# Optimization experiments

Hardware: AMD Instinct MI355X
Metric: run time of the kernel (lower is better)

The kernel has to match this reference:

```python
import jax, jax.numpy as jnp
import numpy as np

N = 20000      # nodes
E = 320000     # edges (before self-loops)
F_IN = 512     # input feature size
HID = 128      # encoder hidden
OUT = 128      # encoder output / GAT in_channels
H = 4          # gat heads
C = 64         # gat out_channels per head


def setup_inputs() -> dict:
    key = jax.random.key(0)
    ks = jax.random.split(key, 10)
    s = 0.05
    return {
        "x": jax.random.normal(ks[0], (N, F_IN), jnp.float32),
        "edge_index": jax.random.randint(ks[1], (2, E), 0, N, dtype=jnp.int64),
        "W1": jax.random.normal(ks[2], (F_IN, HID), jnp.float32) * s,
        "b1": jax.random.normal(ks[3], (HID,), jnp.float32) * s,
        "W2": jax.random.normal(ks[4], (HID, OUT), jnp.float32) * s,
        "b2": jax.random.normal(ks[5], (OUT,), jnp.float32) * s,
        "Wg": jax.random.normal(ks[6], (OUT, H * C), jnp.float32) * s,
        "att_src": jax.random.normal(ks[7], (H, C), jnp.float32) * s,
        "att_dst": jax.random.normal(ks[8], (H, C), jnp.float32) * s,
        "bias_g": jax.random.normal(ks[9], (H * C,), jnp.float32) * s,
    }


def reference(x, edge_index, W1, b1, W2, b2, Wg, att_src, att_dst, bias_g):
    # MLP encoder: Linear -> ReLU -> Linear
    h = jnp.maximum(x @ W1 + b1, 0.0) @ W2 + b2            # [N, OUT]

    # GATConv (concat=True, eval mode -> no dropout)
    xg = (h @ Wg).reshape(N, H, C)                          # per-head projections

    # add self-loops (PyG GATConv default)
    loops = jnp.arange(N, dtype=edge_index.dtype)
    src = jnp.concatenate([edge_index[0], loops])           # [E+N] source j
    dst = jnp.concatenate([edge_index[1], loops])           # [E+N] dest   i

    a_src = jnp.einsum('nhc,hc->nh', xg, att_src)           # [N, H]
    a_dst = jnp.einsum('nhc,hc->nh', xg, att_dst)           # [N, H]

    e = jax.nn.leaky_relu(a_src[src] + a_dst[dst], 0.2)     # [E+N, H]

    # segment softmax over incoming edges of each destination node
    m = jax.ops.segment_max(e, dst, num_segments=N)         # [N, H]
    ex = jnp.exp(e - m[dst])
    denom = jax.ops.segment_sum(ex, dst, num_segments=N)
    alpha = ex / (denom[dst] + 1e-16)                       # [E+N, H]

    # weighted scatter-add aggregation
    out = jax.ops.segment_sum(alpha[:, :, None] * xg[src], dst, num_segments=N)  # [N, H, C]
    return out.reshape(N, H * C) + bias_g
```

## Files before the change

### kernel.cpp

```cpp
#include <hip/hip_runtime.h>
#include <math.h>

#define NNODES 20000
#define NEDGES 320000
#define FIN    512
#define HIDD   128
#define OUTD   128
#define NH     4
#define NC     64
#define HC     256

typedef short bf16x8 __attribute__((ext_vector_type(8)));
typedef float f32x4  __attribute__((ext_vector_type(4)));

__device__ __forceinline__ unsigned short f2bf(float f) {
    unsigned int u = __float_as_uint(f);
    unsigned int r = 0x7fffu + ((u >> 16) & 1u);
    return (unsigned short)((u + r) >> 16);
}
__device__ __forceinline__ float b2f(short t) {
    return __uint_as_float(((unsigned)(unsigned short)t) << 16);
}
__device__ __forceinline__ float4 f4max(float4 a, float4 b) {
    return make_float4(fmaxf(a.x,b.x), fmaxf(a.y,b.y), fmaxf(a.z,b.z), fmaxf(a.w,b.w));
}
__device__ __forceinline__ float4 f4add(float4 a, float4 b) {
    return make_float4(a.x+b.x, a.y+b.y, a.z+b.z, a.w+b.w);
}
__device__ __forceinline__ float4 f4sub(float4 a, float4 b) {
    return make_float4(a.x-b.x, a.y-b.y, a.z-b.z, a.w-b.w);
}
__device__ __forceinline__ float4 f4mul(float4 a, float4 b) {
    return make_float4(a.x*b.x, a.y*b.y, a.z*b.z, a.w*b.w);
}
__device__ __forceinline__ float4 f4exp(float4 a) {
    return make_float4(__expf(a.x), __expf(a.y), __expf(a.z), __expf(a.w));
}
__device__ __forceinline__ float4 shflx4(float4 v, int m) {
    return make_float4(__shfl_xor(v.x,m), __shfl_xor(v.y,m), __shfl_xor(v.z,m), __shfl_xor(v.w,m));
}

__global__ __launch_bounds__(256)
void prep_kernel(const float* __restrict__ W1, unsigned short* __restrict__ W1t,
                 const float* __restrict__ W2, const float* __restrict__ b2,
                 const float* __restrict__ Wg, unsigned short* __restrict__ W2gt,
                 float* __restrict__ b2g, int* __restrict__ deg, int n) {
    const int T1 = FIN * HIDD;
    const int T2 = HC * HIDD;
    int idx = blockIdx.x * 256 + threadIdx.x;
    if (idx < T1) {
        int nn = idx / FIN, k = idx % FIN;
        W1t[idx] = f2bf(W1[(size_t)k * HIDD + nn]);
    } else if (idx < T1 + T2) {
        int local = idx - T1;
        int nn = local >> 7;
        int k  = local & 127;
        float s = 0.f;
        #pragma unroll 8
        for (int t = 0; t < HIDD; ++t)
            s += W2[(size_t)k * OUTD + t] * Wg[(size_t)t * HC + nn];
        W2gt[(size_t)nn * HIDD + k] = f2bf(s);
        if (k == 0) {
            float t2 = 0.f;
            #pragma unroll 8
            for (int t = 0; t < OUTD; ++t) t2 += b2[t] * Wg[(size_t)t * HC + nn];
            b2g[nn] = t2;
        }
    } else if (idx < T1 + T2 + n) {
        deg[idx - T1 - T2] = 1;
    }
}

template<bool A_IS_F32, bool OUT_BF16, int BM>
__global__ __launch_bounds__(256)
void mfma_gemm_kernel(const void* __restrict__ Aptr,
                      const unsigned short* __restrict__ Bt,
                      const float* __restrict__ bias,
                      void* __restrict__ Cptr,
                      int M, int N, int K, int do_relu) {
    constexpr int MF = BM / 32;
    __shared__ unsigned short As[BM * 64];
    __shared__ unsigned short Bs[128 * 64];

    const int tid  = threadIdx.x;
    const int lane = tid & 63;
    const int w    = tid >> 6;
    const int wr   = w >> 1;
    const int wc   = w & 1;
    const int m0   = blockIdx.x * BM;
    const int n0   = blockIdx.y * 128;

    char* pA = (char*)As;
    char* pB = (char*)Bs;

    f32x4 acc[MF][4];
    #pragma unroll
    for (int m = 0; m < MF; ++m)
        #pragma unroll
        for (int n = 0; n < 4; ++n) acc[m][n] = (f32x4){0.f, 0.f, 0.f, 0.f};

    for (int k0 = 0; k0 < K; k0 += 64) {
        if (A_IS_F32) {
            if constexpr (BM == 64) {
                const int row = tid >> 2;
                const int ks  = (tid & 3) << 4;
                const bool ok = (m0 + row) < M;
                const float4* Ap = (const float4*)((const float*)Aptr +
                                   (size_t)(m0 + row) * K + k0 + ks);
                float4 f0 = make_float4(0,0,0,0), f1 = f0, f2 = f0, f3 = f0;
                if (ok) { f0 = Ap[0]; f1 = Ap[1]; f2 = Ap[2]; f3 = Ap[3]; }
                unsigned short u[16];
                u[0]=f2bf(f0.x); u[1]=f2bf(f0.y); u[2]=f2bf(f0.z); u[3]=f2bf(f0.w);
                u[4]=f2bf(f1.x); u[5]=f2bf(f1.y); u[6]=f2bf(f1.z); u[7]=f2bf(f1.w);
                u[8]=f2bf(f2.x); u[9]=f2bf(f2.y); u[10]=f2bf(f2.z); u[11]=f2bf(f2.w);
                u[12]=f2bf(f3.x); u[13]=f2bf(f3.y); u[14]=f2bf(f3.z); u[15]=f2bf(f3.w);
                const int sw = (row & 7) << 4;
                const int base = row * 128 + ks * 2;
                *(bf16x8*)(pA + ((base     ) ^ sw)) = *(bf16x8*)&u[0];
                *(bf16x8*)(pA + ((base + 16) ^ sw)) = *(bf16x8*)&u[8];
            } else {
                const int row = tid >> 3;
                const int sg  = tid & 7;
                const bool ok = (m0 + row) < M;
                const float4* Ap = (const float4*)((const float*)Aptr +
                                   (size_t)(m0 + row) * K + k0 + sg * 8);
                float4 f0 = make_float4(0,0,0,0), f1 = f0;
                if (ok) { f0 = Ap[0]; f1 = Ap[1]; }
                unsigned short u[8];
                u[0]=f2bf(f0.x); u[1]=f2bf(f0.y); u[2]=f2bf(f0.z); u[3]=f2bf(f0.w);
                u[4]=f2bf(f1.x); u[5]=f2bf(f1.y); u[6]=f2bf(f1.z); u[7]=f2bf(f1.w);
                *(bf16x8*)(pA + (((row * 128 + sg * 16)) ^ ((row & 7) << 4))) = *(bf16x8*)&u[0];
            }
        } else {
            const unsigned short* Ab = (const unsigned short*)Aptr;
            #pragma unroll
            for (int i = 0; i < BM / 32; ++i) {
                int s   = tid + i * 256;
                int row = s >> 3;
                int sg  = s & 7;
                bf16x8 v = {};
                if ((m0 + row) < M)
                    v = *(const bf16x8*)(Ab + (size_t)(m0 + row) * K + k0 + sg * 8);
                *(bf16x8*)(pA + (((row * 128 + sg * 16)) ^ ((row & 7) << 4))) = v;
            }
        }
        #pragma unroll
        for (int i = 0; i < 4; ++i) {
            int s   = tid + i * 256;
            int col = s >> 3;
            int sg  = s & 7;
            bf16x8 v = *(const bf16x8*)(Bt + (size_t)(n0 + col) * K + k0 + sg * 8);
            *(bf16x8*)(pB + (((col * 128 + sg * 16)) ^ ((col & 7) << 4))) = v;
        }
        __syncthreads();

        #pragma unroll
        for (int ks = 0; ks < 2; ++ks) {
            const int kb = ks * 64 + ((lane >> 4) << 4);
            bf16x8 a[MF], b[4];
            #pragma unroll
            for (int m = 0; m < MF; ++m) {
                int row = wr * (16 * MF) + m * 16 + (lane & 15);
                a[m] = *(const bf16x8*)(pA + ((row * 128 + kb) ^ ((row & 7) << 4)));
            }
            #pragma unroll
            for (int n = 0; n < 4; ++n) {
                int col = wc * 64 + n * 16 + (lane & 15);
                b[n] = *(const bf16x8*)(pB + ((col * 128 + kb) ^ ((col & 7) << 4)));
            }
            #pragma unroll
            for (int m = 0; m < MF; ++m)
                #pragma unroll
                for (int n = 0; n < 4; ++n)
                    acc[m][n] = __builtin_amdgcn_mfma_f32_16x16x32_bf16(
                        a[m], b[n], acc[m][n], 0, 0, 0);
        }
        __syncthreads();
    }

    #pragma unroll
    for (int n = 0; n < 4; ++n) {
        const int col = n0 + wc * 64 + n * 16 + (lane & 15);
        const float bv = bias ? bias[col] : 0.f;
        #pragma unroll
        for (int m = 0; m < MF; ++m) {
            #pragma unroll
            for (int r = 0; r < 4; ++r) {
                const int row = m0 + wr * (16 * MF) + m * 16 + ((lane >> 4) << 2) + r;
                if (row >= M) continue;
                float v = acc[m][n][r] + bv;
                if (do_relu) v = fmaxf(v, 0.f);
                if (OUT_BF16)
                    ((unsigned short*)Cptr)[(size_t)row * N + col] = f2bf(v);
                else
                    ((float*)Cptr)[(size_t)row * N + col] = v;
            }
        }
    }
}

__global__ __launch_bounds__(256)
void dots_count_kernel(const unsigned short* __restrict__ xgb,
                       const float* __restrict__ att_src, const float* __restrict__ att_dst,
                       float* __restrict__ a_src, float* __restrict__ a_dst,
                       const int* __restrict__ dst, int* __restrict__ deg,
                       int n, int e, int nb_dots) {
    if ((int)blockIdx.x < nb_dots) {
        int idx = blockIdx.x * 256 + threadIdx.x;
        if (idx >= n * NH) return;
        int node = idx >> 2;
        int h = idx & 3;
        const bf16x8* xr = (const bf16x8*)(xgb + (size_t)node * HC + h * NC);
        const float* sa = att_src + h * NC;
        const float* da = att_dst + h * NC;
        float ss = 0.f, dd = 0.f;
        #pragma unroll
        for (int j = 0; j < 8; ++j) {
            bf16x8 v = xr[j];
            #pragma unroll
            for (int t = 0; t < 8; ++t) {
                float f = b2f(v[t]);
                ss += f * sa[j * 8 + t];
                dd += f * da[j * 8 + t];
            }
        }
        a_src[idx] = ss;
        a_dst[idx] = dd;
    } else {
        int i = (blockIdx.x - nb_dots) * 256 + threadIdx.x;
        if (i < e) atomicAdd(&deg[dst[i]], 1);
    }
}

__global__ __launch_bounds__(1024)
void scan_offsets_kernel(const int* __restrict__ deg, int* __restrict__ offs,
                         int* __restrict__ cursor, int n) {
    __shared__ int wsum[16], wbase[16];
    const int tid = threadIdx.x, lane = tid & 63, w = tid >> 6;
    const int i0 = tid * 20;
    int loc[20];
    int s = 0;
    #pragma unroll
    for (int k = 0; k < 20; ++k) {
        int i = i0 + k;
        int v = (i < n) ? deg[i] : 0;
        loc[k] = s;
        s += v;
    }
    int incl = s;
    #pragma unroll
    for (int d = 1; d < 64; d <<= 1) {
        int t = __shfl_up(incl, d);
        if (lane >= d) incl += t;
    }
    if (lane == 63) wsum[w] = incl;
    __syncthreads();
    if (w == 0) {
        int v = (lane < 16) ? wsum[lane] : 0;
        int sc = v;
        #pragma unroll
        for (int d = 1; d < 16; d <<= 1) {
            int t = __shfl_up(sc, d);
            if (lane >= d) sc += t;
        }
        if (lane < 16) wbase[lane] = sc - v;
    }
    __syncthreads();
    const int excl = wbase[w] + incl - s;
    #pragma unroll
    for (int k = 0; k < 20; ++k) {
        int i = i0 + k;
        if (i < n) { int o = excl + loc[k]; offs[i] = o; cursor[i] = o; }
    }
    if (tid == 1023) offs[n] = excl + s;
}

__global__ void scatter_kernel(const int* __restrict__ src, const int* __restrict__ dst,
                               int* __restrict__ cursor, int* __restrict__ csr_src,
                               int e, int n) {
    int i = blockIdx.x * 256 + threadIdx.x;
    if (i < e) {
        int s = src[i], d = dst[i];
        csr_src[atomicAdd(&cursor[d], 1)] = s;
    } else if (i < e + n) {
        int node = i - e;
        csr_src[atomicAdd(&cursor[node], 1)] = node;
    }
}

__global__ __launch_bounds__(256)
void gat_aggregate3_kernel(const unsigned short* __restrict__ xgb,
                           const float4* __restrict__ asrc4,
                           const float4* __restrict__ adst4,
                           const int* __restrict__ offs, const int* __restrict__ csr_src,
                           const float* __restrict__ bias, float* __restrict__ out, int n) {
    __shared__ float4 exbuf[4][64];
    __shared__ int    sbuf[4][64];
    const int wv   = threadIdx.x >> 6;
    const int lane = threadIdx.x & 63;
    const int node = blockIdx.x * 4 + wv;
    if (node >= n) return;
    const int beg = offs[node], end = offs[node + 1];
    const int deg = end - beg;
    const float4 adstv = adst4[node];

    float4 m   = make_float4(-INFINITY, -INFINITY, -INFINITY, -INFINITY);
    float4 den = make_float4(0.f, 0.f, 0.f, 0.f);
    for (int c0 = 0; c0 < deg; c0 += 64) {
        int idx = beg + c0 + lane;
        bool ok = idx < end;
        int s = ok ? csr_src[idx] : 0;
        float4 e = make_float4(-INFINITY, -INFINITY, -INFINITY, -INFINITY);
        if (ok) {
            float4 a = asrc4[s];
            e = f4add(a, adstv);
            e.x = e.x > 0.f ? e.x : 0.2f * e.x;
            e.y = e.y > 0.f ? e.y : 0.2f * e.y;
            e.z = e.z > 0.f ? e.z : 0.2f * e.z;
            e.w = e.w > 0.f ? e.w : 0.2f * e.w;
        }
        float4 cm = e;
        #pragma unroll
        for (int dd = 32; dd >= 1; dd >>= 1) cm = f4max(cm, shflx4(cm, dd));
        float4 nm = f4max(m, cm);
        float4 ex = f4exp(f4sub(e, nm));
        exbuf[wv][lane] = ex;
        sbuf[wv][lane]  = s;
        float4 cs = ex;
        #pragma unroll
        for (int dd = 32; dd >= 1; dd >>= 1) cs = f4add(cs, shflx4(cs, dd));
        den = f4add(f4mul(den, f4exp(f4sub(m, nm))), cs);
        m = nm;
    }

    const int hi = lane >> 5;
    const int ll = lane & 31;
    const int h  = ll >> 3;
    const float denh = (h == 0) ? den.x : (h == 1) ? den.y : (h == 2) ? den.z : den.w;
    const float inv = 1.f / (denh + 1e-16f);

    float4 acc0 = make_float4(0.f, 0.f, 0.f, 0.f);
    float4 acc1 = make_float4(0.f, 0.f, 0.f, 0.f);
    const float* exf = (const float*)&exbuf[wv][0];

    auto do_edge = [&](int jj) {
        int s = sbuf[wv][jj];
        float wgt = exf[jj * 4 + h];
        bf16x8 v = *(const bf16x8*)(xgb + (size_t)s * HC + ll * 8);
        acc0.x += wgt * b2f(v[0]); acc0.y += wgt * b2f(v[1]);
        acc0.z += wgt * b2f(v[2]); acc0.w += wgt * b2f(v[3]);
        acc1.x += wgt * b2f(v[4]); acc1.y += wgt * b2f(v[5]);
        acc1.z += wgt * b2f(v[6]); acc1.w += wgt * b2f(v[7]);
    };

    auto run_chunk = [&](int cn) {
        int j = 0;
        for (; j + 8 <= cn; j += 8) {
            int j0 = j + hi, j1 = j + 2 + hi, j2 = j + 4 + hi, j3 = j + 6 + hi;
            int s0 = sbuf[wv][j0], s1 = sbuf[wv][j1], s2 = sbuf[wv][j2], s3 = sbuf[wv][j3];
            float w0 = exf[j0*4+h], w1 = exf[j1*4+h], w2 = exf[j2*4+h], w3 = exf[j3*4+h];
            bf16x8 v0 = *(const bf16x8*)(xgb + (size_t)s0 * HC + ll * 8);
            bf16x8 v1 = *(const bf16x8*)(xgb + (size_t)s1 * HC + ll * 8);
            bf16x8 v2 = *(const bf16x8*)(xgb + (size_t)s2 * HC + ll * 8);
            bf16x8 v3 = *(const bf16x8*)(xgb + (size_t)s3 * HC + ll * 8);
            acc0.x += w0*b2f(v0[0]); acc0.y += w0*b2f(v0[1]); acc0.z += w0*b2f(v0[2]); acc0.w += w0*b2f(v0[3]);
            acc1.x += w0*b2f(v0[4]); acc1.y += w0*b2f(v0[5]); acc1.z += w0*b2f(v0[6]); acc1.w += w0*b2f(v0[7]);
            acc0.x += w1*b2f(v1[0]); acc0.y += w1*b2f(v1[1]); acc0.z += w1*b2f(v1[2]); acc0.w += w1*b2f(v1[3]);
            acc1.x += w1*b2f(v1[4]); acc1.y += w1*b2f(v1[5]); acc1.z += w1*b2f(v1[6]); acc1.w += w1*b2f(v1[7]);
            acc0.x += w2*b2f(v2[0]); acc0.y += w2*b2f(v2[1]); acc0.z += w2*b2f(v2[2]); acc0.w += w2*b2f(v2[3]);
            acc1.x += w2*b2f(v2[4]); acc1.y += w2*b2f(v2[5]); acc1.z += w2*b2f(v2[6]); acc1.w += w2*b2f(v2[7]);
            acc0.x += w3*b2f(v3[0]); acc0.y += w3*b2f(v3[1]); acc0.z += w3*b2f(v3[2]); acc0.w += w3*b2f(v3[3]);
            acc1.x += w3*b2f(v3[4]); acc1.y += w3*b2f(v3[5]); acc1.z += w3*b2f(v3[6]); acc1.w += w3*b2f(v3[7]);
        }
        for (; j + 4 <= cn; j += 4) {
            do_edge(j + hi);
            do_edge(j + 2 + hi);
        }
        for (; j < cn; j += 2) {
            int jj = j + hi;
            if (jj < cn) do_edge(jj);
        }
    };

    if (deg <= 64) {
        run_chunk(deg);
    } else {
        for (int c0 = 0; c0 < deg; c0 += 64) {
            int idx = beg + c0 + lane;
            if (idx < end) {
                int s = csr_src[idx];
                float4 e = f4add(asrc4[s], adstv);
                e.x = e.x > 0.f ? e.x : 0.2f * e.x;
                e.y = e.y > 0.f ? e.y : 0.2f * e.y;
                e.z = e.z > 0.f ? e.z : 0.2f * e.z;
                e.w = e.w > 0.f ? e.w : 0.2f * e.w;
                exbuf[wv][lane] = f4exp(f4sub(e, m));
                sbuf[wv][lane]  = s;
            }
            int cn = deg - c0; if (cn > 64) cn = 64;
            run_chunk(cn);
        }
    }

    acc0.x += __shfl_xor(acc0.x, 32); acc0.y += __shfl_xor(acc0.y, 32);
    acc0.z += __shfl_xor(acc0.z, 32); acc0.w += __shfl_xor(acc0.w, 32);
    acc1.x += __shfl_xor(acc1.x, 32); acc1.y += __shfl_xor(acc1.y, 32);
    acc1.z += __shfl_xor(acc1.z, 32); acc1.w += __shfl_xor(acc1.w, 32);

    const float4* b4 = (const float4*)bias;
    float4* op = (float4*)(out + (size_t)node * HC);
    if (hi == 0) {
        float4 bv = b4[ll * 2];
        op[ll * 2] = make_float4(acc0.x * inv + bv.x, acc0.y * inv + bv.y,
                                 acc0.z * inv + bv.z, acc0.w * inv + bv.w);
    } else {
        float4 bv = b4[ll * 2 + 1];
        op[ll * 2 + 1] = make_float4(acc1.x * inv + bv.x, acc1.y * inv + bv.y,
                                     acc1.z * inv + bv.z, acc1.w * inv + bv.w);
    }
}

extern "C" void kernel_launch(void* const* d_in, const int* in_sizes, int n_in,
                              void* d_out, int out_size, void* d_ws, size_t ws_size,
                              hipStream_t stream) {
    const float* x       = (const float*)d_in[0];
    const int*   ei      = (const int*)d_in[1];
    const float* W1      = (const float*)d_in[2];
    const float* b1      = (const float*)d_in[3];
    const float* W2      = (const float*)d_in[4];
    const float* b2      = (const float*)d_in[5];
    const float* Wg      = (const float*)d_in[6];
    const float* att_src = (const float*)d_in[7];
    const float* att_dst = (const float*)d_in[8];
    const float* bias_g  = (const float*)d_in[9];

    const int Nn = in_sizes[0] / FIN;
    const int E  = in_sizes[1] / 2;
    const int* e_src = ei;
    const int* e_dst = ei + E;

    char* w = (char*)d_ws;
    auto alloc = [&](size_t bytes) { char* p = w; w += (bytes + 255) & ~(size_t)255; return p; };
    unsigned short* W1t  = (unsigned short*)alloc((size_t)OUTD * FIN * 2);
    unsigned short* W2gt = (unsigned short*)alloc((size_t)HC * HIDD * 2);
    float* b2g  = (float*)alloc(HC * 4);
    unsigned short* h1  = (unsigned short*)alloc((size_t)Nn * HIDD * 2);
    unsigned short* xgb = (unsigned short*)alloc((size_t)Nn * HC * 2);
    float* asrc = (float*)alloc((size_t)Nn * NH * 4);
    float* adst = (float*)alloc((size_t)Nn * NH * 4);
    int* deg    = (int*)alloc((size_t)Nn * 4);
    int* offs   = (int*)alloc((size_t)(Nn + 1) * 4);
    int* cursor = (int*)alloc((size_t)Nn * 4);
    int* csr    = (int*)alloc((size_t)(E + Nn) * 4);

    dim3 blk(256);

    {
        int total = FIN * HIDD + HC * HIDD + Nn;
        prep_kernel<<<dim3((total + 255) / 256), blk, 0, stream>>>(
            W1, W1t, W2, b2, Wg, W2gt, b2g, deg, Nn);
    }

    mfma_gemm_kernel<true, true, 32><<<dim3((Nn + 31) / 32, 1), blk, 0, stream>>>(
        x, W1t, b1, h1, Nn, HIDD, FIN, 1);
    mfma_gemm_kernel<false, true, 64><<<dim3((Nn + 63) / 64, 2), blk, 0, stream>>>(
        h1, W2gt, b2g, xgb, Nn, HC, HIDD, 0);

    {
        int nb_dots = (Nn * NH + 255) / 256;
        int nb_cnt  = (E + 255) / 256;
        dots_count_kernel<<<dim3(nb_dots + nb_cnt), blk, 0, stream>>>(
            xgb, att_src, att_dst, asrc, adst, e_dst, deg, Nn, E, nb_dots);
    }

    scan_offsets_kernel<<<dim3(1), dim3(1024), 0, stream>>>(deg, offs, cursor, Nn);
    scatter_kernel<<<dim3((E + Nn + 255) / 256), blk, 0, stream>>>(
        e_src, e_dst, cursor, csr, E, Nn);

    gat_aggregate3_kernel<<<dim3((Nn + 3) / 4), blk, 0, stream>>>(
        xgb, (const float4*)asrc, (const float4*)adst, offs, csr, bias_g,
        (float*)d_out, Nn);
}
```

Baseline: 130.1 us.

## Fuse attention dots into second GEMM epilogue and degree count into first GEMM

The attention-score dot products are now computed in the epilogue of the second GEMM from fp32 accumulators with a shuffle reduction, which removes a separate kernel that re-read xgb. The edge degree counting moves into the first GEMM launch as extra blocks, so one launch is saved. The aggregation loop also gains a 16-edge unrolled path that issues 8 gathers at once for more memory-level parallelism. The attention dots now use unrounded fp32 values instead of the bf16-stored ones, which slightly changes numerics, and the deeper unroll raises register pressure.

```diff
diff --git a/kernel.cpp b/kernel.cpp
--- a/kernel.cpp
+++ b/kernel.cpp
@@ -71,85 +71,55 @@
     }
 }
 
-template<bool A_IS_F32, bool OUT_BF16, int BM>
 __global__ __launch_bounds__(256)
-void mfma_gemm_kernel(const void* __restrict__ Aptr,
-                      const unsigned short* __restrict__ Bt,
-                      const float* __restrict__ bias,
-                      void* __restrict__ Cptr,
-                      int M, int N, int K, int do_relu) {
-    constexpr int MF = BM / 32;
-    __shared__ unsigned short As[BM * 64];
+void gemm1_count_kernel(const float* __restrict__ A,
+                        const unsigned short* __restrict__ Bt,
+                        const float* __restrict__ bias,
+                        unsigned short* __restrict__ C,
+                        const int* __restrict__ dst, int* __restrict__ deg,
+                        int M, int E, int gemmBlocks) {
+    __shared__ unsigned short As[32 * 64];
     __shared__ unsigned short Bs[128 * 64];
+
+    if ((int)blockIdx.x >= gemmBlocks) {
+        int i = ((int)blockIdx.x - gemmBlocks) * 256 + threadIdx.x;
+        if (i < E) atomicAdd(&deg[dst[i]], 1);
+        return;
+    }
 
     const int tid  = threadIdx.x;
     const int lane = tid & 63;
     const int w    = tid >> 6;
     const int wr   = w >> 1;
     const int wc   = w & 1;
-    const int m0   = blockIdx.x * BM;
-    const int n0   = blockIdx.y * 128;
+    const int m0   = blockIdx.x * 32;
 
     char* pA = (char*)As;
     char* pB = (char*)Bs;
 
-    f32x4 acc[MF][4];
-    #pragma unroll
-    for (int m = 0; m < MF; ++m)
-        #pragma unroll
-        for (int n = 0; n < 4; ++n) acc[m][n] = (f32x4){0.f, 0.f, 0.f, 0.f};
-
-    for (int k0 = 0; k0 < K; k0 += 64) {
-        if (A_IS_F32) {
-            if constexpr (BM == 64) {
-                const int row = tid >> 2;
-                const int ks  = (tid & 3) << 4;
-                const bool ok = (m0 + row) < M;
-                const float4* Ap = (const float4*)((const float*)Aptr +
-                                   (size_t)(m0 + row) * K + k0 + ks);
-                float4 f0 = make_float4(0,0,0,0), f1 = f0, f2 = f0, f3 = f0;
-                if (ok) { f0 = Ap[0]; f1 = Ap[1]; f2 = Ap[2]; f3 = Ap[3]; }
-                unsigned short u[16];
-                u[0]=f2bf(f0.x); u[1]=f2bf(f0.y); u[2]=f2bf(f0.z); u[3]=f2bf(f0.w);
-                u[4]=f2bf(f1.x); u[5]=f2bf(f1.y); u[6]=f2bf(f1.z); u[7]=f2bf(f1.w);
-                u[8]=f2bf(f2.x); u[9]=f2bf(f2.y); u[10]=f2bf(f2.z); u[11]=f2bf(f2.w);
-                u[12]=f2bf(f3.x); u[13]=f2bf(f3.y); u[14]=f2bf(f3.z); u[15]=f2bf(f3.w);
-                const int sw = (row & 7) << 4;
-                const int base = row * 128 + ks * 2;
-                *(bf16x8*)(pA + ((base     ) ^ sw)) = *(bf16x8*)&u[0];
-                *(bf16x8*)(pA + ((base + 16) ^ sw)) = *(bf16x8*)&u[8];
-            } else {
-                const int row = tid >> 3;
-                const int sg  = tid & 7;
-                const bool ok = (m0 + row) < M;
-                const float4* Ap = (const float4*)((const float*)Aptr +
-                                   (size_t)(m0 + row) * K + k0 + sg * 8);
-                float4 f0 = make_float4(0,0,0,0), f1 = f0;
-                if (ok) { f0 = Ap[0]; f1 = Ap[1]; }
-                unsigned short u[8];
-                u[0]=f2bf(f0.x); u[1]=f2bf(f0.y); u[2]=f2bf(f0.z); u[3]=f2bf(f0.w);
-                u[4]=f2bf(f1.x); u[5]=f2bf(f1.y); u[6]=f2bf(f1.z); u[7]=f2bf(f1.w);
-                *(bf16x8*)(pA + (((row * 128 + sg * 16)) ^ ((row & 7) << 4))) = *(bf16x8*)&u[0];
-            }
-        } else {
-            const unsigned short* Ab = (const unsigned short*)Aptr;
-            #pragma unroll
-            for (int i = 0; i < BM / 32; ++i) {
-                int s   = tid + i * 256;
-                int row = s >> 3;
-                int sg  = s & 7;
-                bf16x8 v = {};
-                if ((m0 + row) < M)
-                    v = *(const bf16x8*)(Ab + (size_t)(m0 + row) * K + k0 + sg * 8);
-                *(bf16x8*)(pA + (((row * 128 + sg * 16)) ^ ((row & 7) << 4))) = v;
-            }
+    f32x4 acc[4];
+    #pragma unroll
+    for (int n = 0; n < 4; ++n) acc[n] = (f32x4){0.f, 0.f, 0.f, 0.f};
+
+    for (int k0 = 0; k0 < FIN; k0 += 64) {
+        {
+            const int row = tid >> 3;
+            const int sg  = tid & 7;
+            const bool ok = (m0 + row) < M;
+            const float4* Ap = (const float4*)(A + (size_t)(m0 + row) * FIN + k0 + sg * 8);
+            float4 f0 = make_float4(0,0,0,0), f1 = f0;
+            if (ok) { f0 = Ap[0]; f1 = Ap[1]; }
+            unsigned short u[8];
+            u[0]=f2bf(f0.x); u[1]=f2bf(f0.y); u[2]=f2bf(f0.z); u[3]=f2bf(f0.w);
+            u[4]=f2bf(f1.x); u[5]=f2bf(f1.y); u[6]=f2bf(f1.z); u[7]=f2bf(f1.w);
+            *(bf16x8*)(pA + (((row * 128 + sg * 16)) ^ ((row & 7) << 4))) = *(bf16x8*)&u[0];
         }
         #pragma unroll
         for (int i = 0; i < 4; ++i) {
             int s   = tid + i * 256;
             int col = s >> 3;
             int sg  = s & 7;
-            bf16x8 v = *(const bf16x8*)(Bt + (size_t)(n0 + col) * K + k0 + sg * 8);
+            bf16x8 v = *(const bf16x8*)(Bt + (size_t)col * FIN + k0 + sg * 8);
             *(bf16x8*)(pB + (((col * 128 + sg * 16)) ^ ((col & 7) << 4))) = v;
         }
         __syncthreads();
@@ -157,19 +127,101 @@
         #pragma unroll
         for (int ks = 0; ks < 2; ++ks) {
             const int kb = ks * 64 + ((lane >> 4) << 4);
-            bf16x8 a[MF], b[4];
-            #pragma unroll
-            for (int m = 0; m < MF; ++m) {
-                int row = wr * (16 * MF) + m * 16 + (lane & 15);
-                a[m] = *(const bf16x8*)(pA + ((row * 128 + kb) ^ ((row & 7) << 4)));
-            }
+            int row = wr * 16 + (lane & 15);
+            bf16x8 a = *(const bf16x8*)(pA + ((row * 128 + kb) ^ ((row & 7) << 4)));
+            bf16x8 b[4];
             #pragma unroll
             for (int n = 0; n < 4; ++n) {
                 int col = wc * 64 + n * 16 + (lane & 15);
                 b[n] = *(const bf16x8*)(pB + ((col * 128 + kb) ^ ((col & 7) << 4)));
             }
             #pragma unroll
-            for (int m = 0; m < MF; ++m)
+            for (int n = 0; n < 4; ++n)
+                acc[n] = __builtin_amdgcn_mfma_f32_16x16x32_bf16(a, b[n], acc[n], 0, 0, 0);
+        }
+        __syncthreads();
+    }
+
+    #pragma unroll
+    for (int n = 0; n < 4; ++n) {
+        const int col = wc * 64 + n * 16 + (lane & 15);
+        const float bv = bias[col];
+        #pragma unroll
+        for (int r = 0; r < 4; ++r) {
+            const int row = m0 + wr * 16 + ((lane >> 4) << 2) + r;
+            if (row >= M) continue;
+            float v = fmaxf(acc[n][r] + bv, 0.f);
+            C[(size_t)row * HIDD + col] = f2bf(v);
+        }
+    }
+}
+
+__global__ __launch_bounds__(256)
+void gemm2_dots_kernel(const unsigned short* __restrict__ Ab,
+                       const unsigned short* __restrict__ Bt,
+                       const float* __restrict__ b2g,
+                       const float* __restrict__ att_src,
+                       const float* __restrict__ att_dst,
+                       unsigned short* __restrict__ xgb,
+                       float* __restrict__ a_src, float* __restrict__ a_dst,
+                       int M) {
+    __shared__ unsigned short As[64 * 64];
+    __shared__ unsigned short Bs[128 * 64];
+
+    const int tid  = threadIdx.x;
+    const int lane = tid & 63;
+    const int w    = tid >> 6;
+    const int wr   = w >> 1;
+    const int wc   = w & 1;
+    const int m0   = blockIdx.x * 64;
+    const int n0   = blockIdx.y * 128;
+
+    char* pA = (char*)As;
+    char* pB = (char*)Bs;
+
+    f32x4 acc[2][4];
+    #pragma unroll
+    for (int m = 0; m < 2; ++m)
+        #pragma unroll
+        for (int n = 0; n < 4; ++n) acc[m][n] = (f32x4){0.f, 0.f, 0.f, 0.f};
+
+    for (int k0 = 0; k0 < HIDD; k0 += 64) {
+        #pragma unroll
+        for (int i = 0; i < 2; ++i) {
+            int s   = tid + i * 256;
+            int row = s >> 3;
+            int sg  = s & 7;
+            bf16x8 v = {};
+            if ((m0 + row) < M)
+                v = *(const bf16x8*)(Ab + (size_t)(m0 + row) * HIDD + k0 + sg * 8);
+            *(bf16x8*)(pA + (((row * 128 + sg * 16)) ^ ((row & 7) << 4))) = v;
+        }
+        #pragma unroll
+        for (int i = 0; i < 4; ++i) {
+            int s   = tid + i * 256;
+            int col = s >> 3;
+            int sg  = s & 7;
+            bf16x8 v = *(const bf16x8*)(Bt + (size_t)(n0 + col) * HIDD + k0 + sg * 8);
+            *(bf16x8*)(pB + (((col * 128 + sg * 16)) ^ ((col & 7) << 4))) = v;
+        }
+        __syncthreads();
+
+        #pragma unroll
+        for (int ks = 0; ks < 2; ++ks) {
+            const int kb = ks * 64 + ((lane >> 4) << 4);
+            bf16x8 a[2], b[4];
+            #pragma unroll
+            for (int m = 0; m < 2; ++m) {
+                int row = wr * 32 + m * 16 + (lane & 15);
+                a[m] = *(const bf16x8*)(pA + ((row * 128 + kb) ^ ((row & 7) << 4)));
+            }
+            #pragma unroll
+            for (int n = 0; n < 4; ++n) {
+                int col = wc * 64 + n * 16 + (lane & 15);
+                b[n] = *(const bf16x8*)(pB + ((col * 128 + kb) ^ ((col & 7) << 4)));
+            }
+            #pragma unroll
+            for (int m = 0; m < 2; ++m)
                 #pragma unroll
                 for (int n = 0; n < 4; ++n)
                     acc[m][n] = __builtin_amdgcn_mfma_f32_16x16x32_bf16(
@@ -178,57 +230,50 @@
         __syncthreads();
     }
 
+    const int head = blockIdx.y * 2 + wc;
+    const int cIn  = lane & 15;
+    float ds_p[2][4], dd_p[2][4];
+    #pragma unroll
+    for (int m = 0; m < 2; ++m)
+        #pragma unroll
+        for (int r = 0; r < 4; ++r) { ds_p[m][r] = 0.f; dd_p[m][r] = 0.f; }
+
     #pragma unroll
     for (int n = 0; n < 4; ++n) {
-        const int col = n0 + wc * 64 + n * 16 + (lane & 15);
-        const float bv = bias ? bias[col] : 0.f;
-        #pragma unroll
-        for (int m = 0; m < MF; ++m) {
+        const int ch  = n * 16 + cIn;
+        const int col = n0 + wc * 64 + n * 16 + cIn;
+        const float bv   = b2g[col];
+        const float as_c = att_src[head * NC + ch];
+        const float ad_c = att_dst[head * NC + ch];
+        #pragma unroll
+        for (int m = 0; m < 2; ++m) {
             #pragma unroll
             for (int r = 0; r < 4; ++r) {
-                const int row = m0 + wr * (16 * MF) + m * 16 + ((lane >> 4) << 2) + r;
-                if (row >= M) continue;
+                const int row = m0 + wr * 32 + m * 16 + ((lane >> 4) << 2) + r;
                 float v = acc[m][n][r] + bv;
-                if (do_relu) v = fmaxf(v, 0.f);
-                if (OUT_BF16)
-                    ((unsigned short*)Cptr)[(size_t)row * N + col] = f2bf(v);
-                else
-                    ((float*)Cptr)[(size_t)row * N + col] = v;
-            }
-        }
-    }
-}
-
-__global__ __launch_bounds__(256)
-void dots_count_kernel(const unsigned short* __restrict__ xgb,
-                       const float* __restrict__ att_src, const float* __restrict__ att_dst,
-                       float* __restrict__ a_src, float* __restrict__ a_dst,
-                       const int* __restrict__ dst, int* __restrict__ deg,
-                       int n, int e, int nb_dots) {
-    if ((int)blockIdx.x < nb_dots) {
-        int idx = blockIdx.x * 256 + threadIdx.x;
-        if (idx >= n * NH) return;
-        int node = idx >> 2;
-        int h = idx & 3;
-        const bf16x8* xr = (const bf16x8*)(xgb + (size_t)node * HC + h * NC);
-        const float* sa = att_src + h * NC;
-        const float* da = att_dst + h * NC;
-        float ss = 0.f, dd = 0.f;
-        #pragma unroll
-        for (int j = 0; j < 8; ++j) {
-            bf16x8 v = xr[j];
-            #pragma unroll
-            for (int t = 0; t < 8; ++t) {
-                float f = b2f(v[t]);
-                ss += f * sa[j * 8 + t];
-                dd += f * da[j * 8 + t];
-            }
-        }
-        a_src[idx] = ss;
-        a_dst[idx] = dd;
-    } else {
-        int i = (blockIdx.x - nb_dots) * 256 + threadIdx.x;
-        if (i < e) atomicAdd(&deg[dst[i]], 1);
+                if (row < M) xgb[(size_t)row * HC + col] = f2bf(v);
+                ds_p[m][r] += v * as_c;
+                dd_p[m][r] += v * ad_c;
+            }
+        }
+    }
+    #pragma unroll
+    for (int m = 0; m < 2; ++m) {
+        #pragma unroll
+        for (int r = 0; r < 4; ++r) {
+            float s = ds_p[m][r], d = dd_p[m][r];
+            s += __shfl_xor(s, 1); s += __shfl_xor(s, 2);
+            s += __shfl_xor(s, 4); s += __shfl_xor(s, 8);
+            d += __shfl_xor(d, 1); d += __shfl_xor(d, 2);
+            d += __shfl_xor(d, 4); d += __shfl_xor(d, 8);
+            if (cIn == 0) {
+                const int row = m0 + wr * 32 + m * 16 + ((lane >> 4) << 2) + r;
+                if (row < M) {
+                    a_src[row * NH + head] = s;
+                    a_dst[row * NH + head] = d;
+                }
+            }
+        }
     }
 }
 
@@ -289,7 +334,7 @@
 }
 
 __global__ __launch_bounds__(256)
-void gat_aggregate3_kernel(const unsigned short* __restrict__ xgb,
+void gat_aggregate4_kernel(const unsigned short* __restrict__ xgb,
                            const float4* __restrict__ asrc4,
                            const float4* __restrict__ adst4,
                            const int* __restrict__ offs, const int* __restrict__ csr_src,
@@ -355,22 +400,28 @@
 
     auto run_chunk = [&](int cn) {
         int j = 0;
+        for (; j + 16 <= cn; j += 16) {
+            int ss[8]; float ww[8]; bf16x8 vv[8];
+            #pragma unroll
+            for (int t = 0; t < 8; ++t) {
+                int jj = j + 2 * t + hi;
+                ss[t] = sbuf[wv][jj];
+                ww[t] = exf[jj * 4 + h];
+            }
+            #pragma unroll
+            for (int t = 0; t < 8; ++t)
+                vv[t] = *(const bf16x8*)(xgb + (size_t)ss[t] * HC + ll * 8);
+            #pragma unroll
+            for (int t = 0; t < 8; ++t) {
+                acc0.x += ww[t]*b2f(vv[t][0]); acc0.y += ww[t]*b2f(vv[t][1]);
+                acc0.z += ww[t]*b2f(vv[t][2]); acc0.w += ww[t]*b2f(vv[t][3]);
+                acc1.x += ww[t]*b2f(vv[t][4]); acc1.y += ww[t]*b2f(vv[t][5]);
+                acc1.z += ww[t]*b2f(vv[t][6]); acc1.w += ww[t]*b2f(vv[t][7]);
+            }
+        }
         for (; j + 8 <= cn; j += 8) {
-            int j0 = j + hi, j1 = j + 2 + hi, j2 = j + 4 + hi, j3 = j + 6 + hi;
-            int s0 = sbuf[wv][j0], s1 = sbuf[wv][j1], s2 = sbuf[wv][j2], s3 = sbuf[wv][j3];
-            float w0 = exf[j0*4+h], w1 = exf[j1*4+h], w2 = exf[j2*4+h], w3 = exf[j3*4+h];
-            bf16x8 v0 = *(const bf16x8*)(xgb + (size_t)s0 * HC + ll * 8);
-            bf16x8 v1 = *(const bf16x8*)(xgb + (size_t)s1 * HC + ll * 8);
-            bf16x8 v2 = *(const bf16x8*)(xgb + (size_t)s2 * HC + ll * 8);
-            bf16x8 v3 = *(const bf16x8*)(xgb + (size_t)s3 * HC + ll * 8);
-            acc0.x += w0*b2f(v0[0]); acc0.y += w0*b2f(v0[1]); acc0.z += w0*b2f(v0[2]); acc0.w += w0*b2f(v0[3]);
-            acc1.x += w0*b2f(v0[4]); acc1.y += w0*b2f(v0[5]); acc1.z += w0*b2f(v0[6]); acc1.w += w0*b2f(v0[7]);
-            acc0.x += w1*b2f(v1[0]); acc0.y += w1*b2f(v1[1]); acc0.z += w1*b2f(v1[2]); acc0.w += w1*b2f(v1[3]);
-            acc1.x += w1*b2f(v1[4]); acc1.y += w1*b2f(v1[5]); acc1.z += w1*b2f(v1[6]); acc1.w += w1*b2f(v1[7]);
-            acc0.x += w2*b2f(v2[0]); acc0.y += w2*b2f(v2[1]); acc0.z += w2*b2f(v2[2]); acc0.w += w2*b2f(v2[3]);
-            acc1.x += w2*b2f(v2[4]); acc1.y += w2*b2f(v2[5]); acc1.z += w2*b2f(v2[6]); acc1.w += w2*b2f(v2[7]);
-            acc0.x += w3*b2f(v3[0]); acc0.y += w3*b2f(v3[1]); acc0.z += w3*b2f(v3[2]); acc0.w += w3*b2f(v3[3]);
-            acc1.x += w3*b2f(v3[4]); acc1.y += w3*b2f(v3[5]); acc1.z += w3*b2f(v3[6]); acc1.w += w3*b2f(v3[7]);
+            do_edge(j + hi);     do_edge(j + 2 + hi);
+            do_edge(j + 4 + hi); do_edge(j + 6 + hi);
         }
         for (; j + 4 <= cn; j += 4) {
             do_edge(j + hi);
@@ -461,23 +512,21 @@
             W1, W1t, W2, b2, Wg, W2gt, b2g, deg, Nn);
     }
 
-    mfma_gemm_kernel<true, true, 32><<<dim3((Nn + 31) / 32, 1), blk, 0, stream>>>(
-        x, W1t, b1, h1, Nn, HIDD, FIN, 1);
-    mfma_gemm_kernel<false, true, 64><<<dim3((Nn + 63) / 64, 2), blk, 0, stream>>>(
-        h1, W2gt, b2g, xgb, Nn, HC, HIDD, 0);
-
     {
-        int nb_dots = (Nn * NH + 255) / 256;
-        int nb_cnt  = (E + 255) / 256;
-        dots_count_kernel<<<dim3(nb_dots + nb_cnt), blk, 0, stream>>>(
-            xgb, att_src, att_dst, asrc, adst, e_dst, deg, Nn, E, nb_dots);
-    }
+        int gb = (Nn + 31) / 32;
+        int cb = (E + 255) / 256;
+        gemm1_count_kernel<<<dim3(gb + cb), blk, 0, stream>>>(
+            x, W1t, b1, h1, e_dst, deg, Nn, E, gb);
+    }
+
+    gemm2_dots_kernel<<<dim3((Nn + 63) / 64, 2), blk, 0, stream>>>(
+        h1, W2gt, b2g, att_src, att_dst, xgb, asrc, adst, Nn);
 
     scan_offsets_kernel<<<dim3(1), dim3(1024), 0, stream>>>(deg, offs, cursor, Nn);
     scatter_kernel<<<dim3((E + Nn + 255) / 256), blk, 0, stream>>>(
         e_src, e_dst, cursor, csr, E, Nn);
 
-    gat_aggregate3_kernel<<<dim3((Nn + 3) / 4), blk, 0, stream>>>(
+    gat_aggregate4_kernel<<<dim3((Nn + 3) / 4), blk, 0, stream>>>(
         xgb, (const float4*)asrc, (const float4*)adst, offs, csr, bias_g,
         (float*)d_out, Nn);
 }
```

New measurement: 127.0 us. 2.4% less time.
